# Kernel tuning notes

Measured on AMD Instinct MI355X. Metric: run time of the kernel, lower is better.

## Reference

```python
import jax, jax.numpy as jnp
import numpy as np

D_MODEL = 512
D_STATE = 64
HEADDIM = 64
EXPAND = 2
D_CONV = 4
D_INNER = EXPAND * D_MODEL            # 1024
NHEADS = D_INNER // HEADDIM           # 16
CONV_DIM = D_INNER + 2 * D_STATE      # 1152 (x, B, C share the depthwise conv)
D_IN_PROJ = 2 * D_INNER + 2 * D_STATE + NHEADS  # z, xBC, dt
C_IN = 512


def setup_inputs() -> dict:
    key = jax.random.key(0)
    ks = jax.random.split(key, 10)
    hs = jax.random.normal(ks[0], (1, C_IN, 16, 16, 16), jnp.float32)
    return {
        "hidden_states": hs,
        # 1x1 conv projections (weight stored as (out,in))
        "proj_in_w": jax.random.normal(ks[1], (D_MODEL, C_IN), jnp.float32) / np.float32(np.sqrt(C_IN)),
        "proj_in_b": jnp.zeros((D_MODEL,), jnp.float32),
        "proj_out_w": jax.random.normal(ks[2], (C_IN, D_MODEL), jnp.float32) * jnp.float32(0.02),
        "proj_out_b": jnp.zeros((C_IN,), jnp.float32),
        # Mamba2 core params
        "in_proj_w": jax.random.normal(ks[3], (D_IN_PROJ, D_MODEL), jnp.float32) / np.float32(np.sqrt(D_MODEL)),
        "conv_w": jax.random.normal(ks[4], (CONV_DIM, D_CONV), jnp.float32) / np.float32(np.sqrt(D_CONV)),
        "conv_b": jnp.zeros((CONV_DIM,), jnp.float32),
        "dt_bias": jnp.log(jnp.expm1(jax.random.uniform(ks[5], (NHEADS,), jnp.float32, 1e-3, 0.1))),
        "A_log": jnp.log(jax.random.uniform(ks[6], (NHEADS,), jnp.float32, 1.0, 16.0)),
        "D": jnp.ones((NHEADS,), jnp.float32),
        "norm_w": jnp.ones((D_INNER,), jnp.float32),
        "out_proj_w": jax.random.normal(ks[7], (D_MODEL, D_INNER), jnp.float32) / np.float32(np.sqrt(D_INNER)),
    }


def _mamba2(x, in_proj_w, conv_w, conv_b, dt_bias, A_log, Dp, norm_w, out_proj_w):
    # x: (N, T, d_model) with N = B*H*W (independent pixel sequences over time)
    N, T, _ = x.shape
    zxbcdt = jnp.einsum('ntd,ed->nte', x, in_proj_w)  # (N,T,D_IN_PROJ)
    z = zxbcdt[..., :D_INNER]
    xBC = zxbcdt[..., D_INNER:D_INNER + CONV_DIM]
    dt = zxbcdt[..., D_INNER + CONV_DIM:]             # (N,T,NHEADS)
    # causal depthwise conv along T (kernel D_CONV, left-padded), then SiLU
    pad = jnp.pad(xBC, ((0, 0), (D_CONV - 1, 0), (0, 0)))
    xc = sum(pad[:, k:k + T, :] * conv_w[:, k] for k in range(D_CONV))
    xBC = jax.nn.silu(xc + conv_b)
    xs = xBC[..., :D_INNER].reshape(N, T, NHEADS, HEADDIM)
    Bm = xBC[..., D_INNER:D_INNER + D_STATE]          # (N,T,D_STATE), ngroups=1
    Cm = xBC[..., D_INNER + D_STATE:]                 # (N,T,D_STATE)
    dt = jax.nn.softplus(dt + dt_bias)                # (N,T,NHEADS)
    A = -jnp.exp(A_log)                               # (NHEADS,)

    def step(h, inp):
        # h: (N, NHEADS, HEADDIM, D_STATE)
        dt_t, x_t, B_t, C_t = inp
        dA = jnp.exp(dt_t * A)                        # (N,NHEADS)
        h = h * dA[:, :, None, None] + (dt_t[:, :, None] * x_t)[..., None] * B_t[:, None, None, :]
        y_t = jnp.einsum('nhps,ns->nhp', h, C_t)      # (N,NHEADS,HEADDIM)
        return h, y_t

    h0 = jnp.zeros((N, NHEADS, HEADDIM, D_STATE), x.dtype)
    _, ys = jax.lax.scan(step, h0, (dt.swapaxes(0, 1), xs.swapaxes(0, 1), Bm.swapaxes(0, 1), Cm.swapaxes(0, 1)))
    y = ys.swapaxes(0, 1) + Dp[None, None, :, None] * xs   # skip term
    # gated RMSNorm: norm(y * silu(z)) * weight
    y = y.reshape(N, T, D_INNER) * jax.nn.silu(z)
    y = y * jax.lax.rsqrt(jnp.mean(y * y, axis=-1, keepdims=True) + 1e-5) * norm_w
    return jnp.einsum('ntd,od->nto', y, out_proj_w)


def reference(hidden_states, proj_in_w, proj_in_b, proj_out_w, proj_out_b,
              in_proj_w, conv_w, conv_b, dt_bias, A_log, D, norm_w, out_proj_w):
    B, C, T, H, W = hidden_states.shape
    # proj_in: 1x1 conv over channels == per-pixel matmul
    x = jnp.einsum('bcthw,dc->bthwd', hidden_states, proj_in_w) + proj_in_b
    # (B,T,H,W,D) -> (B*H*W, T, D): each pixel becomes a temporal sequence
    x = x.transpose(0, 2, 3, 1, 4).reshape(B * H * W, T, D_MODEL)
    y = _mamba2(x, in_proj_w, conv_w, conv_b, dt_bias, A_log, D, norm_w, out_proj_w)
    y = y.reshape(B, H, W, T, D_MODEL).transpose(0, 3, 1, 2, 4)  # (B,T,H,W,D)
    out = jnp.einsum('bthwd,cd->bcthw', y, proj_out_w) + proj_out_b[None, :, None, None, None]
    return (out,)
```

## Files before the change

### kernel.cpp

```cpp
#include <hip/hip_runtime.h>
#include <hip/hip_bf16.h>
#include <math.h>

#define TT       16
#define NSEQ     256
#define TOK      4096
#define DMODEL   512
#define DINNER   1024
#define DSTATE   64
#define NHEADS   16
#define HEADDIM  64
#define CONVDIM  1152
#define DINPROJ  2192
#define DTOFF    2176
#define ZLD      2176
#define NPAD_IP  2304

using bf16x8 = __attribute__((ext_vector_type(8))) short;
using f32x4  = __attribute__((ext_vector_type(4))) float;
typedef __hip_bfloat16 bf16;

__device__ __forceinline__ void gload_lds16(const void* g, void* l) {
    __builtin_amdgcn_global_load_lds(
        (const __attribute__((address_space(1))) unsigned int*)g,
        (__attribute__((address_space(3))) unsigned int*)l,
        16, 0, 0);
}

template<int NFRAG, bool OUTBF, bool DUAL, int BIAS, bool SCALEROW>
__global__ __launch_bounds__(256) void mfma_gemm(
    const bf16* __restrict__ A, const bf16* __restrict__ B,
    const float* __restrict__ bias, const float* __restrict__ rs,
    float* __restrict__ Cf, bf16* __restrict__ Ch, float* __restrict__ C2,
    int Nreal, int K, int lda, int ldb, int ldc)
{
    constexpr int BN = NFRAG * 32;
    __shared__ short As[128 * 32];
    __shared__ short Bs[BN * 32];

    const int tid = threadIdx.x;
    const int wv = tid >> 6, ln = tid & 63;
    const int m0 = blockIdx.x * 128, n0 = blockIdx.y * BN;
    const int wr = wv >> 1, wc = wv & 1;
    const int lr = ln & 15, lk = (ln >> 4) * 8;

    f32x4 acc[4][NFRAG];
#pragma unroll
    for (int m = 0; m < 4; ++m)
#pragma unroll
        for (int n = 0; n < NFRAG; ++n) acc[m][n] = (f32x4){0.f, 0.f, 0.f, 0.f};

    for (int k0 = 0; k0 < K; k0 += 32) {
        __syncthreads();
#pragma unroll
        for (int r = 0; r < 2; ++r) {
            const int ofs = r * 4096 + tid * 16;
            const int row = ofs >> 6;
            const int ke  = (ofs & 63) >> 1;
            gload_lds16(A + (size_t)(m0 + row) * lda + k0 + ke, (char*)As + ofs);
        }
#pragma unroll
        for (int r = 0; r < NFRAG / 2; ++r) {
            const int ofs = r * 4096 + tid * 16;
            const int row = ofs >> 6;
            const int ke  = (ofs & 63) >> 1;
            gload_lds16(B + (size_t)(n0 + row) * ldb + k0 + ke, (char*)Bs + ofs);
        }
        __syncthreads();

        bf16x8 af[4], bfr[NFRAG];
#pragma unroll
        for (int m = 0; m < 4; ++m)
            af[m] = *(const bf16x8*)&As[(wr * 64 + m * 16 + lr) * 32 + lk];
#pragma unroll
        for (int n = 0; n < NFRAG; ++n)
            bfr[n] = *(const bf16x8*)&Bs[(wc * (BN / 2) + n * 16 + lr) * 32 + lk];
#pragma unroll
        for (int m = 0; m < 4; ++m)
#pragma unroll
            for (int n = 0; n < NFRAG; ++n)
                acc[m][n] = __builtin_amdgcn_mfma_f32_16x16x32_bf16(
                    af[m], bfr[n], acc[m][n], 0, 0, 0);
    }

    const int mBase = m0 + wr * 64, nBase = n0 + wc * (BN / 2);
#pragma unroll
    for (int m = 0; m < 4; ++m) {
#pragma unroll
        for (int n = 0; n < NFRAG; ++n) {
            const int col = nBase + n * 16 + lr;
            if (col < Nreal) {
#pragma unroll
                for (int j = 0; j < 4; ++j) {
                    const int row = mBase + m * 16 + (ln >> 4) * 4 + j;
                    float v = acc[m][n][j];
                    if (BIAS == 1) v += bias[col];
                    if (BIAS == 2) v += bias[row];
                    if (SCALEROW) v *= rs[row];
                    if (OUTBF) {
                        Ch[(size_t)row * ldc + col] = __float2bfloat16(v);
                        if (DUAL) C2[(size_t)row * ldc + col] = v;
                    } else {
                        Cf[(size_t)row * ldc + col] = v;
                    }
                }
            }
        }
    }
}

#define SZ_PI  (512 * 512)
#define SZ_PO  (512 * 512)
#define SZ_OP  (512 * 1024)
#define SZ_IP  (DINPROJ * 512)
#define SZ_IPP (NPAD_IP * 512)
#define SZ_ALL (SZ_PI + SZ_PO + SZ_OP + SZ_IPP)

__global__ __launch_bounds__(256) void prep_weights(
    const float* __restrict__ pi, const float* __restrict__ po,
    const float* __restrict__ op, const float* __restrict__ ip,
    const float* __restrict__ nw,
    bf16* __restrict__ wpi, bf16* __restrict__ wpo,
    bf16* __restrict__ wop, bf16* __restrict__ wip)
{
    for (int idx = blockIdx.x * 256 + threadIdx.x; idx < SZ_ALL;
         idx += gridDim.x * 256) {
        if (idx < SZ_PI) {
            wpi[idx] = __float2bfloat16(pi[idx]);
        } else if (idx < SZ_PI + SZ_PO) {
            int j = idx - SZ_PI; wpo[j] = __float2bfloat16(po[j]);
        } else if (idx < SZ_PI + SZ_PO + SZ_OP) {
            int j = idx - SZ_PI - SZ_PO;
            wop[j] = __float2bfloat16(op[j] * nw[j & 1023]);
        } else {
            int j = idx - SZ_PI - SZ_PO - SZ_OP;
            wip[j] = (j < SZ_IP) ? __float2bfloat16(ip[j]) : __float2bfloat16(0.f);
        }
    }
}

__global__ __launch_bounds__(256) void transpose_hs(
    const float* __restrict__ hs, bf16* __restrict__ hsT)
{
    __shared__ float tile[32][33];
    const int v0 = blockIdx.x * 32, c0 = blockIdx.y * 32;
    const int tx = threadIdx.x, ty = threadIdx.y;
#pragma unroll
    for (int i = 0; i < 4; ++i)
        tile[ty + 8 * i][tx] = hs[(size_t)(c0 + ty + 8 * i) * TOK + v0 + tx];
    __syncthreads();
#pragma unroll
    for (int i = 0; i < 4; ++i)
        hsT[(size_t)(v0 + ty + 8 * i) * DMODEL + c0 + tx] =
            __float2bfloat16(tile[tx][ty + 8 * i]);
}

__global__ __launch_bounds__(256) void dt_fix_kernel(
    const float* __restrict__ xv32, const float* __restrict__ in_proj_w,
    float* __restrict__ dtf)
{
    const int v = blockIdx.x;
    const int w = threadIdx.x >> 6, l = threadIdx.x & 63;
    const float4* xr = (const float4*)(xv32 + (size_t)v * DMODEL);
    const float4 x0 = xr[l * 2], x1 = xr[l * 2 + 1];
#pragma unroll
    for (int hh = 0; hh < 4; ++hh) {
        const int h = w * 4 + hh;
        const float4* wr = (const float4*)(in_proj_w + (size_t)(DTOFF + h) * DMODEL);
        const float4 w0 = wr[l * 2], w1 = wr[l * 2 + 1];
        float dot = x0.x * w0.x + x0.y * w0.y + x0.z * w0.z + x0.w * w0.w
                  + x1.x * w1.x + x1.y * w1.y + x1.z * w1.z + x1.w * w1.w;
#pragma unroll
        for (int off = 32; off >= 1; off >>= 1) dot += __shfl_xor(dot, off);
        if (l == 0) dtf[(size_t)v * 16 + h] = dot;
    }
}

__global__ __launch_bounds__(256) void ssd_kernel(
    const bf16* __restrict__ zb, const float* __restrict__ dtf,
    const float* __restrict__ conv_w, const float* __restrict__ conv_b,
    const float* __restrict__ dt_bias, const float* __restrict__ A_log,
    const float* __restrict__ Dp,
    bf16* __restrict__ gb, float* __restrict__ part)
{
    const int n = blockIdx.x, hq = blockIdx.y;
    const int tid = threadIdx.x;
    const int w = tid >> 6, p = tid & 63;
    const int h = hq * 4 + w;
    const int ch = hq * 256 + tid;

    __shared__ float Bsh[16][68];
    __shared__ float Csh[16][68];
    __shared__ float Gsh[16][16];
    __shared__ float Msh[4][256];
    __shared__ float red4[16][4];

    float ld[16];
#pragma unroll
    for (int t = 0; t < 16; ++t)
        ld[t] = __bfloat162float(zb[(size_t)(t * 256 + n) * ZLD + 1024 + ch]);

    const float cw0 = conv_w[ch * 4 + 0], cw1 = conv_w[ch * 4 + 1],
                cw2 = conv_w[ch * 4 + 2], cw3 = conv_w[ch * 4 + 3];
    const float cb = conv_b[ch];
    float xs[16];
#pragma unroll
    for (int t = 0; t < 16; ++t) {
        float a = fmaf(ld[t], cw3, cb);
        if (t >= 1) a = fmaf(ld[t - 1], cw2, a);
        if (t >= 2) a = fmaf(ld[t - 2], cw1, a);
        if (t >= 3) a = fmaf(ld[t - 3], cw0, a);
        xs[t] = a / (1.f + __expf(-a));
    }

    if (tid < 128) {
        const int cc = 1024 + tid;
        const float dw0 = conv_w[cc * 4 + 0], dw1 = conv_w[cc * 4 + 1],
                    dw2 = conv_w[cc * 4 + 2], dw3 = conv_w[cc * 4 + 3];
        const float db = conv_b[cc];
        float q0 = 0.f, q1 = 0.f, q2 = 0.f;
#pragma unroll
        for (int t = 0; t < 16; ++t) {
            const float cur =
                __bfloat162float(zb[(size_t)(t * 256 + n) * ZLD + 2048 + tid]);
            float a = fmaf(cur, dw3, db);
            a = fmaf(q2, dw2, a);
            a = fmaf(q1, dw1, a);
            a = fmaf(q0, dw0, a);
            const float val = a / (1.f + __expf(-a));
            if (tid < 64) Bsh[t][tid] = val; else Csh[t][tid - 64] = val;
            q0 = q1; q1 = q2; q2 = cur;
        }
    }

    const float a_h = -__expf(A_log[h]);
    float dtv_l = 0.f;
    if (p < 16) {
        const float raw = dtf[(size_t)(p * 256 + n) * 16 + h] + dt_bias[h];
        dtv_l = (raw > 20.f) ? raw : log1pf(__expf(raw));
    }
    float cum_l = dtv_l;
#pragma unroll
    for (int off = 1; off < 16; off <<= 1) {
        const float tmp = __shfl_up(cum_l, off);
        if (p >= off) cum_l += tmp;
    }
    __syncthreads();

    {
        const int t = tid >> 4, s = tid & 15;
        float acc = 0.f;
#pragma unroll
        for (int k = 0; k < 64; ++k)
            acc = fmaf(Csh[t][k], Bsh[s][k], acc);
        Gsh[t][s] = acc;
    }
    __syncthreads();

    float dtv_all[16], cum_all[16];
#pragma unroll
    for (int t = 0; t < 16; ++t) {
        dtv_all[t] = __shfl(dtv_l, t);
        cum_all[t] = __shfl(cum_l, t);
    }
#pragma unroll
    for (int q = 0; q < 4; ++q) {
        const int idx = p * 4 + q;
        const int t = idx >> 4, s = idx & 15;
        float m = 0.f;
        if (s <= t)
            m = __expf(a_h * (cum_all[t] - cum_all[s])) * Gsh[t][s] * dtv_all[s];
        Msh[w][idx] = m;
    }

    float zl[16];
#pragma unroll
    for (int t = 0; t < 16; ++t)
        zl[t] = __bfloat162float(zb[(size_t)(t * 256 + n) * ZLD + ch]);

    const float Dh = Dp[h];
    float g[16];
#pragma unroll
    for (int t = 0; t < 16; ++t) {
        float y = 0.f;
#pragma unroll
        for (int s = 0; s <= t; ++s)
            y = fmaf(Msh[w][t * 16 + s], xs[s], y);
        y = fmaf(Dh, xs[t], y);
        g[t] = y * (zl[t] / (1.f + __expf(-zl[t])));
    }

#pragma unroll
    for (int t = 0; t < 16; ++t) {
        float ss = g[t] * g[t];
#pragma unroll
        for (int off = 32; off >= 1; off >>= 1) ss += __shfl_xor(ss, off);
        if (p == 0) red4[t][w] = ss;
        gb[(size_t)(t * 256 + n) * DINNER + ch] = __float2bfloat16(g[t]);
    }
    __syncthreads();
    if (tid < 16)
        part[(size_t)(tid * 256 + n) * 4 + hq] =
            red4[tid][0] + red4[tid][1] + red4[tid][2] + red4[tid][3];
}

__global__ __launch_bounds__(256) void scale_kernel(
    const float* __restrict__ part, float* __restrict__ scalev)
{
    const int v = blockIdx.x * 256 + threadIdx.x;
    const float4 pv = *(const float4*)(part + (size_t)v * 4);
    const float s = pv.x + pv.y + pv.z + pv.w;
    scalev[v] = rsqrtf(s * (1.f / 1024.f) + 1e-5f);
}

extern "C" void kernel_launch(void* const* d_in, const int* in_sizes, int n_in,
                              void* d_out, int out_size, void* d_ws, size_t ws_size,
                              hipStream_t stream) {
    const float* hs         = (const float*)d_in[0];
    const float* proj_in_w  = (const float*)d_in[1];
    const float* proj_in_b  = (const float*)d_in[2];
    const float* proj_out_w = (const float*)d_in[3];
    const float* proj_out_b = (const float*)d_in[4];
    const float* in_proj_w  = (const float*)d_in[5];
    const float* conv_w     = (const float*)d_in[6];
    const float* conv_b     = (const float*)d_in[7];
    const float* dt_bias    = (const float*)d_in[8];
    const float* A_log      = (const float*)d_in[9];
    const float* Dp         = (const float*)d_in[10];
    const float* norm_w     = (const float*)d_in[11];
    const float* out_proj_w = (const float*)d_in[12];
    float* out = (float*)d_out;

    float* ws      = (float*)d_ws;
    float* xv32    = ws;
    float* dtf     = xv32 + (size_t)TOK * DMODEL;
    float* part    = dtf + (size_t)TOK * 16;
    float* scalev  = part + (size_t)TOK * 4;
    bf16*  hsT     = (bf16*)(scalev + TOK);
    bf16*  xv_bf   = hsT + (size_t)TOK * DMODEL;
    bf16*  zb      = xv_bf + (size_t)TOK * DMODEL;
    bf16*  gb      = zb + (size_t)TOK * ZLD;
    bf16*  y2      = gb + (size_t)TOK * DINNER;
    bf16*  wpi     = y2 + (size_t)TOK * DMODEL;
    bf16*  wpo     = wpi + SZ_PI;
    bf16*  wop     = wpo + SZ_PO;
    bf16*  wip     = wop + SZ_OP;

    prep_weights<<<1024, 256, 0, stream>>>(proj_in_w, proj_out_w, out_proj_w,
                                           in_proj_w, norm_w, wpi, wpo, wop, wip);
    transpose_hs<<<dim3(128, 16), dim3(32, 8), 0, stream>>>(hs, hsT);

    mfma_gemm<2, true, true, 1, false><<<dim3(32, 8), 256, 0, stream>>>(
        hsT, wpi, proj_in_b, nullptr, nullptr, xv_bf, xv32,
        DMODEL, DMODEL, DMODEL, DMODEL, DMODEL);

    mfma_gemm<4, true, false, 0, false><<<dim3(32, 18), 256, 0, stream>>>(
        xv_bf, wip, nullptr, nullptr, nullptr, zb, nullptr,
        ZLD, DMODEL, DMODEL, DMODEL, ZLD);

    dt_fix_kernel<<<TOK, 256, 0, stream>>>(xv32, in_proj_w, dtf);

    ssd_kernel<<<dim3(NSEQ, 4), 256, 0, stream>>>(
        zb, dtf, conv_w, conv_b, dt_bias, A_log, Dp, gb, part);

    scale_kernel<<<dim3(TOK / 256), 256, 0, stream>>>(part, scalev);

    mfma_gemm<2, true, false, 0, true><<<dim3(32, 8), 256, 0, stream>>>(
        gb, wop, nullptr, scalev, nullptr, y2, nullptr,
        DMODEL, DINNER, DINNER, DINNER, DMODEL);

    mfma_gemm<2, false, false, 2, false><<<dim3(4, 64), 256, 0, stream>>>(
        wpo, y2, proj_out_b, nullptr, out, nullptr, nullptr,
        TOK, DMODEL, DMODEL, DMODEL, TOK);
}
```

Before: 118.5 us.

## Fold dt projection into proj_in weights, merge prep kernels, fuse RMS scale into GEMM

The in_proj dt rows are precomposed with proj_in (Wc = W_dt·W_pi, bc = W_dt·b_pi), so dt is computed directly from hs in fp32. This removes the fp32 copy of the proj_in output and the per-token dt_fix launch. The weight prep and hs transpose are merged into one launch that also builds Wc. The RMSNorm scale kernel is removed by computing rsqrt from the partial sums inside the out_proj GEMM epilogue. In exchange, the new dt kernel does a strided 512-deep scalar loop over hs with only 64 blocks, and 16 prep blocks each run a serial 512-length reduction.

```diff
diff --git a/kernel.cpp b/kernel.cpp
--- a/kernel.cpp
+++ b/kernel.cpp
@@ -27,11 +27,11 @@
         16, 0, 0);
 }
 
-template<int NFRAG, bool OUTBF, bool DUAL, int BIAS, bool SCALEROW>
+template<int NFRAG, bool OUTBF, int BIAS, bool PARTSCALE>
 __global__ __launch_bounds__(256) void mfma_gemm(
     const bf16* __restrict__ A, const bf16* __restrict__ B,
     const float* __restrict__ bias, const float* __restrict__ rs,
-    float* __restrict__ Cf, bf16* __restrict__ Ch, float* __restrict__ C2,
+    float* __restrict__ Cf, bf16* __restrict__ Ch,
     int Nreal, int K, int lda, int ldb, int ldc)
 {
     constexpr int BN = NFRAG * 32;
@@ -87,22 +87,24 @@
 #pragma unroll
     for (int m = 0; m < 4; ++m) {
 #pragma unroll
-        for (int n = 0; n < NFRAG; ++n) {
-            const int col = nBase + n * 16 + lr;
-            if (col < Nreal) {
-#pragma unroll
-                for (int j = 0; j < 4; ++j) {
-                    const int row = mBase + m * 16 + (ln >> 4) * 4 + j;
+        for (int j = 0; j < 4; ++j) {
+            const int row = mBase + m * 16 + (ln >> 4) * 4 + j;
+            float sc = 1.f, rb = 0.f;
+            if (PARTSCALE) {
+                const float4 pv = *(const float4*)(rs + (size_t)row * 4);
+                sc = rsqrtf((pv.x + pv.y + pv.z + pv.w) * (1.f / 1024.f) + 1e-5f);
+            }
+            if (BIAS == 2) rb = bias[row];
+#pragma unroll
+            for (int n = 0; n < NFRAG; ++n) {
+                const int col = nBase + n * 16 + lr;
+                if (col < Nreal) {
                     float v = acc[m][n][j];
                     if (BIAS == 1) v += bias[col];
-                    if (BIAS == 2) v += bias[row];
-                    if (SCALEROW) v *= rs[row];
-                    if (OUTBF) {
-                        Ch[(size_t)row * ldc + col] = __float2bfloat16(v);
-                        if (DUAL) C2[(size_t)row * ldc + col] = v;
-                    } else {
-                        Cf[(size_t)row * ldc + col] = v;
-                    }
+                    v += rb;
+                    if (PARTSCALE) v *= sc;
+                    if (OUTBF) Ch[(size_t)row * ldc + col] = __float2bfloat16(v);
+                    else       Cf[(size_t)row * ldc + col] = v;
                 }
             }
         }
@@ -115,65 +117,89 @@
 #define SZ_IP  (DINPROJ * 512)
 #define SZ_IPP (NPAD_IP * 512)
 #define SZ_ALL (SZ_PI + SZ_PO + SZ_OP + SZ_IPP)
-
-__global__ __launch_bounds__(256) void prep_weights(
+#define PREP_WB 512
+#define PREP_TB 2048
+
+__global__ __launch_bounds__(256) void prep_all(
     const float* __restrict__ pi, const float* __restrict__ po,
     const float* __restrict__ op, const float* __restrict__ ip,
-    const float* __restrict__ nw,
+    const float* __restrict__ nw, const float* __restrict__ pib,
+    const float* __restrict__ hs,
     bf16* __restrict__ wpi, bf16* __restrict__ wpo,
-    bf16* __restrict__ wop, bf16* __restrict__ wip)
+    bf16* __restrict__ wop, bf16* __restrict__ wip,
+    float* __restrict__ Wc, float* __restrict__ bc, bf16* __restrict__ hsT)
 {
-    for (int idx = blockIdx.x * 256 + threadIdx.x; idx < SZ_ALL;
-         idx += gridDim.x * 256) {
-        if (idx < SZ_PI) {
-            wpi[idx] = __float2bfloat16(pi[idx]);
-        } else if (idx < SZ_PI + SZ_PO) {
-            int j = idx - SZ_PI; wpo[j] = __float2bfloat16(po[j]);
-        } else if (idx < SZ_PI + SZ_PO + SZ_OP) {
-            int j = idx - SZ_PI - SZ_PO;
-            wop[j] = __float2bfloat16(op[j] * nw[j & 1023]);
-        } else {
-            int j = idx - SZ_PI - SZ_PO - SZ_OP;
-            wip[j] = (j < SZ_IP) ? __float2bfloat16(ip[j]) : __float2bfloat16(0.f);
-        }
-    }
-}
-
-__global__ __launch_bounds__(256) void transpose_hs(
-    const float* __restrict__ hs, bf16* __restrict__ hsT)
+    __shared__ float smem[32 * 33];
+    const int b = blockIdx.x, tid = threadIdx.x;
+
+    if (b < PREP_WB) {
+        for (int idx = b * 256 + tid; idx < SZ_ALL; idx += PREP_WB * 256) {
+            if (idx < SZ_PI) {
+                wpi[idx] = __float2bfloat16(pi[idx]);
+            } else if (idx < SZ_PI + SZ_PO) {
+                int j = idx - SZ_PI; wpo[j] = __float2bfloat16(po[j]);
+            } else if (idx < SZ_PI + SZ_PO + SZ_OP) {
+                int j = idx - SZ_PI - SZ_PO;
+                wop[j] = __float2bfloat16(op[j] * nw[j & 1023]);
+            } else {
+                int j = idx - SZ_PI - SZ_PO - SZ_OP;
+                wip[j] = (j < SZ_IP) ? __float2bfloat16(ip[j])
+                                     : __float2bfloat16(0.f);
+            }
+        }
+    } else if (b < PREP_WB + PREP_TB) {
+        const int tb = b - PREP_WB;
+        const int v0 = (tb & 127) * 32, c0 = (tb >> 7) * 32;
+        const int tx = tid & 31, ty = tid >> 5;
+#pragma unroll
+        for (int i = 0; i < 4; ++i)
+            smem[(ty + 8 * i) * 33 + tx] =
+                hs[(size_t)(c0 + ty + 8 * i) * TOK + v0 + tx];
+        __syncthreads();
+#pragma unroll
+        for (int i = 0; i < 4; ++i)
+            hsT[(size_t)(v0 + ty + 8 * i) * DMODEL + c0 + tx] =
+                __float2bfloat16(smem[tx * 33 + ty + 8 * i]);
+    } else {
+        const int h = b - PREP_WB - PREP_TB;
+        const float* wdt = ip + (size_t)(DTOFF + h) * DMODEL;
+#pragma unroll
+        for (int rep = 0; rep < 2; ++rep) {
+            const int c = tid + rep * 256;
+            float acc = 0.f;
+            for (int d = 0; d < 512; ++d)
+                acc = fmaf(wdt[d], pi[(size_t)d * DMODEL + c], acc);
+            Wc[(size_t)h * DMODEL + c] = acc;
+        }
+        float p = pib[tid] * wdt[tid] + pib[tid + 256] * wdt[tid + 256];
+#pragma unroll
+        for (int off = 32; off >= 1; off >>= 1) p += __shfl_xor(p, off);
+        if ((tid & 63) == 0) smem[tid >> 6] = p;
+        __syncthreads();
+        if (tid == 0) bc[h] = smem[0] + smem[1] + smem[2] + smem[3];
+    }
+}
+
+__global__ __launch_bounds__(256) void dt_direct_kernel(
+    const float* __restrict__ hs, const float* __restrict__ Wc,
+    const float* __restrict__ bc, float* __restrict__ dtf)
 {
-    __shared__ float tile[32][33];
-    const int v0 = blockIdx.x * 32, c0 = blockIdx.y * 32;
-    const int tx = threadIdx.x, ty = threadIdx.y;
-#pragma unroll
-    for (int i = 0; i < 4; ++i)
-        tile[ty + 8 * i][tx] = hs[(size_t)(c0 + ty + 8 * i) * TOK + v0 + tx];
-    __syncthreads();
-#pragma unroll
-    for (int i = 0; i < 4; ++i)
-        hsT[(size_t)(v0 + ty + 8 * i) * DMODEL + c0 + tx] =
-            __float2bfloat16(tile[tx][ty + 8 * i]);
-}
-
-__global__ __launch_bounds__(256) void dt_fix_kernel(
-    const float* __restrict__ xv32, const float* __restrict__ in_proj_w,
-    float* __restrict__ dtf)
-{
-    const int v = blockIdx.x;
-    const int w = threadIdx.x >> 6, l = threadIdx.x & 63;
-    const float4* xr = (const float4*)(xv32 + (size_t)v * DMODEL);
-    const float4 x0 = xr[l * 2], x1 = xr[l * 2 + 1];
-#pragma unroll
-    for (int hh = 0; hh < 4; ++hh) {
-        const int h = w * 4 + hh;
-        const float4* wr = (const float4*)(in_proj_w + (size_t)(DTOFF + h) * DMODEL);
-        const float4 w0 = wr[l * 2], w1 = wr[l * 2 + 1];
-        float dot = x0.x * w0.x + x0.y * w0.y + x0.z * w0.z + x0.w * w0.w
-                  + x1.x * w1.x + x1.y * w1.y + x1.z * w1.z + x1.w * w1.w;
-#pragma unroll
-        for (int off = 32; off >= 1; off >>= 1) dot += __shfl_xor(dot, off);
-        if (l == 0) dtf[(size_t)v * 16 + h] = dot;
-    }
+    const int v = blockIdx.x * 64 + (threadIdx.x & 63);
+    const int hq = threadIdx.x >> 6;
+    const float* w0 = Wc + (size_t)(hq * 4 + 0) * DMODEL;
+    const float* w1 = Wc + (size_t)(hq * 4 + 1) * DMODEL;
+    const float* w2 = Wc + (size_t)(hq * 4 + 2) * DMODEL;
+    const float* w3 = Wc + (size_t)(hq * 4 + 3) * DMODEL;
+    float a0 = 0.f, a1 = 0.f, a2 = 0.f, a3 = 0.f;
+#pragma unroll 8
+    for (int c = 0; c < 512; ++c) {
+        const float x = hs[(size_t)c * TOK + v];
+        a0 = fmaf(x, w0[c], a0); a1 = fmaf(x, w1[c], a1);
+        a2 = fmaf(x, w2[c], a2); a3 = fmaf(x, w3[c], a3);
+    }
+    float4 r = make_float4(a0 + bc[hq * 4 + 0], a1 + bc[hq * 4 + 1],
+                           a2 + bc[hq * 4 + 2], a3 + bc[hq * 4 + 3]);
+    *(float4*)(dtf + (size_t)v * 16 + hq * 4) = r;
 }
 
 __global__ __launch_bounds__(256) void ssd_kernel(
@@ -302,15 +328,6 @@
     if (tid < 16)
         part[(size_t)(tid * 256 + n) * 4 + hq] =
             red4[tid][0] + red4[tid][1] + red4[tid][2] + red4[tid][3];
-}
-
-__global__ __launch_bounds__(256) void scale_kernel(
-    const float* __restrict__ part, float* __restrict__ scalev)
-{
-    const int v = blockIdx.x * 256 + threadIdx.x;
-    const float4 pv = *(const float4*)(part + (size_t)v * 4);
-    const float s = pv.x + pv.y + pv.z + pv.w;
-    scalev[v] = rsqrtf(s * (1.f / 1024.f) + 1e-5f);
 }
 
 extern "C" void kernel_launch(void* const* d_in, const int* in_sizes, int n_in,
@@ -332,11 +349,11 @@
     float* out = (float*)d_out;
 
     float* ws      = (float*)d_ws;
-    float* xv32    = ws;
-    float* dtf     = xv32 + (size_t)TOK * DMODEL;
+    float* dtf     = ws;
     float* part    = dtf + (size_t)TOK * 16;
-    float* scalev  = part + (size_t)TOK * 4;
-    bf16*  hsT     = (bf16*)(scalev + TOK);
+    float* Wc      = part + (size_t)TOK * 4;
+    float* bc      = Wc + 16 * DMODEL;
+    bf16*  hsT     = (bf16*)(bc + 16);
     bf16*  xv_bf   = hsT + (size_t)TOK * DMODEL;
     bf16*  zb      = xv_bf + (size_t)TOK * DMODEL;
     bf16*  gb      = zb + (size_t)TOK * ZLD;
@@ -346,30 +363,28 @@
     bf16*  wop     = wpo + SZ_PO;
     bf16*  wip     = wop + SZ_OP;
 
-    prep_weights<<<1024, 256, 0, stream>>>(proj_in_w, proj_out_w, out_proj_w,
-                                           in_proj_w, norm_w, wpi, wpo, wop, wip);
-    transpose_hs<<<dim3(128, 16), dim3(32, 8), 0, stream>>>(hs, hsT);
-
-    mfma_gemm<2, true, true, 1, false><<<dim3(32, 8), 256, 0, stream>>>(
-        hsT, wpi, proj_in_b, nullptr, nullptr, xv_bf, xv32,
+    prep_all<<<PREP_WB + PREP_TB + 16, 256, 0, stream>>>(
+        proj_in_w, proj_out_w, out_proj_w, in_proj_w, norm_w, proj_in_b, hs,
+        wpi, wpo, wop, wip, Wc, bc, hsT);
+
+    mfma_gemm<2, true, 1, false><<<dim3(32, 8), 256, 0, stream>>>(
+        hsT, wpi, proj_in_b, nullptr, nullptr, xv_bf,
         DMODEL, DMODEL, DMODEL, DMODEL, DMODEL);
 
-    mfma_gemm<4, true, false, 0, false><<<dim3(32, 18), 256, 0, stream>>>(
-        xv_bf, wip, nullptr, nullptr, nullptr, zb, nullptr,
+    mfma_gemm<4, true, 0, false><<<dim3(32, 18), 256, 0, stream>>>(
+        xv_bf, wip, nullptr, nullptr, nullptr, zb,
         ZLD, DMODEL, DMODEL, DMODEL, ZLD);
 
-    dt_fix_kernel<<<TOK, 256, 0, stream>>>(xv32, in_proj_w, dtf);
+    dt_direct_kernel<<<64, 256, 0, stream>>>(hs, Wc, bc, dtf);
 
     ssd_kernel<<<dim3(NSEQ, 4), 256, 0, stream>>>(
         zb, dtf, conv_w, conv_b, dt_bias, A_log, Dp, gb, part);
 
-    scale_kernel<<<dim3(TOK / 256), 256, 0, stream>>>(part, scalev);
-
-    mfma_gemm<2, true, false, 0, true><<<dim3(32, 8), 256, 0, stream>>>(
-        gb, wop, nullptr, scalev, nullptr, y2, nullptr,
+    mfma_gemm<2, true, 0, true><<<dim3(32, 8), 256, 0, stream>>>(
+        gb, wop, nullptr, part, nullptr, y2,
         DMODEL, DINNER, DINNER, DINNER, DMODEL);
 
-    mfma_gemm<2, false, false, 2, false><<<dim3(4, 64), 256, 0, stream>>>(
-        wpo, y2, proj_out_b, nullptr, out, nullptr, nullptr,
+    mfma_gemm<2, false, 2, false><<<dim3(4, 64), 256, 0, stream>>>(
+        wpo, y2, proj_out_b, nullptr, out, nullptr,
         TOK, DMODEL, DMODEL, DMODEL, TOK);
 }
```

Measured after the change: 170.0 us. +43.5%, slower.
